# Optimization experiments

Hardware: AMD Instinct MI355X
Metric: run time of the kernel (lower is better)

## Reference

```python
import jax, jax.numpy as jnp
import numpy as np

COMMIT_WEIGHT = 0.25  # cfg.commit_weight


def setup_inputs() -> dict:
    key = jax.random.key(0)
    k1, k2 = jax.random.split(key)
    z = jax.random.normal(k1, (262144, 64), dtype=jnp.float32)
    codebook = jax.random.normal(k2, (512, 64), dtype=jnp.float32) * 0.02
    return {"z": z, "codebook": codebook}


def reference(z, codebook):
    # projector = Identity (apply_sim_vq=False)
    # squared euclidean distances [N, K]; argmin matches cdist(p=2) argmin
    d2 = (
        jnp.sum(z * z, axis=-1, keepdims=True)
        - 2.0 * (z @ codebook.T)
        + jnp.sum(codebook * codebook, axis=-1)
    )
    ids = jnp.argmin(d2, axis=-1)          # [N] int
    q = codebook[ids]                       # [N, D] gather
    loss = (
        jnp.mean((jax.lax.stop_gradient(z) - q) ** 2)
        + COMMIT_WEIGHT * jnp.mean((jax.lax.stop_gradient(q) - z) ** 2)
    )
    # straight-through estimator (training path)
    q_ste = z + jax.lax.stop_gradient(q - z)
    return q_ste, loss, ids
```

## Files before the change

kernel.cpp:

```cpp
#include <hip/hip_runtime.h>
#include <math.h>


constexpr int D     = 64;
constexpr int D4    = 16;
constexpr int K     = 512;
constexpr float STH = 2e-4f;

typedef __attribute__((ext_vector_type(8)))  short s16x8;
typedef __attribute__((ext_vector_type(16))) float f32x16;

#define FMA4(acc, zz, cc) do { \
  acc = fmaf((zz).x, (cc).x, acc); \
  acc = fmaf((zz).y, (cc).y, acc); \
  acc = fmaf((zz).z, (cc).z, acc); \
  acc = fmaf((zz).w, (cc).w, acc); } while (0)

#define MFMA_B(A, B, C) __builtin_amdgcn_mfma_f32_32x32x16_bf16(A, B, C, 0, 0, 0)

__device__ __forceinline__ unsigned short f2bf(float f) {
  unsigned u = __float_as_uint(f);
  return (unsigned short)((u + 0x7FFFu + ((u >> 16) & 1u)) >> 16);
}


#define LDS_FRAGS(CH, CL, T) do { \
  const int fb_ = (T) * 4096 + h * 512 + col * 16; \
  CH[0] = *(const s16x8*)(smem + fb_); \
  CH[1] = *(const s16x8*)(smem + fb_ + 1024); \
  CH[2] = *(const s16x8*)(smem + fb_ + 2048); \
  CH[3] = *(const s16x8*)(smem + fb_ + 3072); \
  CL[0] = *(const s16x8*)(smem + 65536 + fb_); \
  CL[1] = *(const s16x8*)(smem + 65536 + fb_ + 1024); \
  CL[2] = *(const s16x8*)(smem + 65536 + fb_ + 2048); \
  CL[3] = *(const s16x8*)(smem + 65536 + fb_ + 3072); \
} while (0)

#define LDS_GG(G, T) do { \
  const int gb_ = 131072 + (((T) * 32 + h * 16) << 2); \
  G[0] = *(const float4*)(smem + gb_); \
  G[1] = *(const float4*)(smem + gb_ + 16); \
  G[2] = *(const float4*)(smem + gb_ + 32); \
  G[3] = *(const float4*)(smem + gb_ + 48); \
} while (0)

#define TILE_BODY(T, CH, CL, G) do { \
  f32x16 acc0, acc1 = {};             \
  acc0[0]  = G[0].x; acc0[1]  = G[0].y; acc0[2]  = G[0].z; acc0[3]  = G[0].w; \
  acc0[4]  = G[1].x; acc0[5]  = G[1].y; acc0[6]  = G[1].z; acc0[7]  = G[1].w; \
  acc0[8]  = G[2].x; acc0[9]  = G[2].y; acc0[10] = G[2].z; acc0[11] = G[2].w; \
  acc0[12] = G[3].x; acc0[13] = G[3].y; acc0[14] = G[3].z; acc0[15] = G[3].w; \
  acc0 = MFMA_B(CH[0], zh[0], acc0);  acc1 = MFMA_B(CH[1], zh[1], acc1); \
  acc0 = MFMA_B(CH[2], zh[2], acc0);  acc1 = MFMA_B(CH[3], zh[3], acc1); \
  acc0 = MFMA_B(CH[0], zl[0], acc0);  acc1 = MFMA_B(CH[1], zl[1], acc1); \
  acc0 = MFMA_B(CH[2], zl[2], acc0);  acc1 = MFMA_B(CH[3], zl[3], acc1); \
  acc0 = MFMA_B(CL[0], zh[0], acc0);  acc1 = MFMA_B(CL[1], zh[1], acc1); \
  acc0 = MFMA_B(CL[2], zh[2], acc0);  acc1 = MFMA_B(CL[3], zh[3], acc1); \
   \
  float m1a = -INFINITY, m2a = -INFINITY, m1b = -INFINITY, m2b = -INFINITY; \
  int ra_ = 0, rb_ = 8; \
  _Pragma("unroll") \
  for (int r = 0; r < 8; ++r) { \
    float v = acc0[r] + acc1[r];        \
    bool gt = v > m1a;                  \
    m2a = fminf(fmaxf(v, m2a), m1a);    \
    if (gt) ra_ = r; \
    m1a = gt ? v : m1a; \
  } \
  _Pragma("unroll") \
  for (int r = 8; r < 16; ++r) { \
    float v = acc0[r] + acc1[r]; \
    bool gt = v > m1b; \
    m2b = fminf(fmaxf(v, m2b), m1b); \
    if (gt) rb_ = r; \
    m1b = gt ? v : m1b; \
  } \
   \
  float tm1 = fmaxf(m1a, m1b); \
  float tm2 = fmaxf(fminf(m1a, m1b), fmaxf(m2a, m2b)); \
  int   tr_ = (m1b > m1a) ? rb_ : ra_;    \
  bool tgt = tm1 > m1;                    \
  m2 = fmaxf(fminf(tm1, m1), fmaxf(tm2, m2)); \
  if (tgt) { rbest = tr_; tbest = (T); } \
  m1 = tgt ? tm1 : m1; \
} while (0)

__global__ __launch_bounds__(512, 2)
void vq_main(const float* __restrict__ z, const float* __restrict__ cbk,
             float* __restrict__ out, float* __restrict__ lossAcc,
             unsigned* __restrict__ done, int N)
{
  extern __shared__ char smem[];

  const int tid  = threadIdx.x;
  const int lane = tid & 63;
  const int wave = tid >> 6;
  const int col  = lane & 31;
  const int h    = lane >> 5;

  {
    const int cw = tid;
    const float4* c4 = (const float4*)(cbk + (size_t)cw * D);
    float4 f[16];
    #pragma unroll
    for (int i = 0; i < D4; ++i) f[i] = c4[i];
    float c2 = 0.f;
    #pragma unroll
    for (int i = 0; i < D4; ++i) FMA4(c2, f[i], f[i]);
    float e[64];
    #pragma unroll
    for (int i = 0; i < D4; ++i) {
      e[4*i] = f[i].x; e[4*i+1] = f[i].y; e[4*i+2] = f[i].z; e[4*i+3] = f[i].w;
    }
    const int T = cw >> 5, cc = cw & 31;
    #pragma unroll
    for (int sl = 0; sl < 4; ++sl) {
      #pragma unroll
      for (int h2 = 0; h2 < 2; ++h2) {
        const int ld0 = sl * 16 + h2 * 8;
        s16x8 vh, vl;
        #pragma unroll
        for (int j = 0; j < 8; ++j) {
          unsigned short hb = f2bf(e[ld0 + j]);
          float hf = __uint_as_float((unsigned)hb << 16);
          vh[j] = (short)hb;
          vl[j] = (short)f2bf(e[ld0 + j] - hf);
        }
        const int a = T * 4096 + sl * 1024 + h2 * 512 + cc * 16;
        *(s16x8*)(smem + a) = vh;
        *(s16x8*)(smem + 65536 + a) = vl;
      }
    }
    const int ai = (T << 5) + (((cc >> 2) & 1) << 4) + ((cc >> 3) << 2) + (cc & 3);
    *(float*)(smem + 131072 + ai * 4) = -0.5f * c2;
  }
  __syncthreads();

  float lacc = 0.f;

  #pragma unroll 1
  for (int it = 0; it < 4; ++it) {
    const long rowg = (long)blockIdx.x * 1024 + it * 256 + wave * 32 + col;

    const float4* zp4 = (const float4*)(z + (size_t)rowg * D);
    s16x8 zh[4], zl[4];
    #pragma unroll
    for (int s = 0; s < 4; ++s) {
      float4 p0 = zp4[4 * s + 2 * h];
      float4 p1 = zp4[4 * s + 2 * h + 1];
      float e[8] = {p0.x, p0.y, p0.z, p0.w, p1.x, p1.y, p1.z, p1.w};
      #pragma unroll
      for (int j = 0; j < 8; ++j) {
        unsigned short hb = f2bf(e[j]);
        float hf = __uint_as_float((unsigned)hb << 16);
        zh[s][j] = (short)hb;
        zl[s][j] = (short)f2bf(e[j] - hf);
      }
    }

    float m1 = -INFINITY, m2 = -INFINITY;
    int rbest = 0, tbest = 0;

    s16x8 chA[4], clA[4], chB[4], clB[4];
    float4 gA[4], gB[4];
    LDS_FRAGS(chA, clA, 0);  LDS_GG(gA, 0);
    LDS_FRAGS(chB, clB, 1);  LDS_GG(gB, 1);
    #pragma unroll 1
    for (int t = 0; t < 14; t += 2) {
      TILE_BODY(t, chA, clA, gA);
      LDS_FRAGS(chA, clA, t + 2);  LDS_GG(gA, t + 2);
      TILE_BODY(t + 1, chB, clB, gB);
      LDS_FRAGS(chB, clB, t + 3);  LDS_GG(gB, t + 3);
    }
    TILE_BODY(14, chA, clA, gA);
    TILE_BODY(15, chB, clB, gB);

    int idx = (tbest << 5) + (h << 2) + (rbest & 3) + ((rbest >> 2) << 3);

    float om1  = __shfl_xor(m1, 32);
    float om2  = __shfl_xor(m2, 32);
    int   oidx = __shfl_xor(idx, 32);
    float nm2 = fmaxf(fminf(m1, om1), fmaxf(m2, om2));
    bool take = (om1 > m1) || ((om1 == m1) && (oidx < idx));
    if (take) { m1 = om1; idx = oidx; }
    m2 = nm2;

    const bool certain = (m1 - m2 > STH);
    if (certain) {
      const float4* qp = (const float4*)(cbk + (size_t)idx * D) + (h << 3);
      const float4* zp = (const float4*)(z + (size_t)rowg * D) + (h << 3);
      float4*       op = (float4*)(out + (size_t)rowg * D) + (h << 3);
      #pragma unroll
      for (int i = 0; i < 8; ++i) {
        float4 q = qp[i], zz = zp[i], u, qs;
        u.x = q.x - zz.x; u.y = q.y - zz.y; u.z = q.z - zz.z; u.w = q.w - zz.w;
        qs.x = zz.x + u.x; qs.y = zz.y + u.y; qs.z = zz.z + u.z; qs.w = zz.w + u.w;
        FMA4(lacc, u, u);
        op[i] = qs;
      }
      if (h == 0) (out + (size_t)N * D + 1)[rowg] = (float)idx;
    }

    unsigned mask32 = (unsigned)__ballot((!certain) && h == 0);
    while (mask32) {
      const int c = __builtin_ctz(mask32);
      mask32 &= mask32 - 1;
      const size_t r0 = (size_t)blockIdx.x * 1024 + it * 256 + wave * 32 + c;
      const float4* zp = (const float4*)(z + r0 * D);
      float4 z0[D4];
      #pragma unroll
      for (int i = 0; i < D4; ++i) z0[i] = zp[i];
      float z2 = 0.f;
      #pragma unroll
      for (int i = 0; i < D4; ++i) FMA4(z2, z0[i], z0[i]);

      float best = INFINITY;
      int   bi = 0;
      #pragma unroll 1
      for (int j = 0; j < 8; ++j) {
        const int k = (lane << 3) + j;
        const float4* c4 = (const float4*)(cbk + (size_t)k * D);
        float4 cr[D4];
        #pragma unroll
        for (int i = 0; i < D4; ++i) cr[i] = c4[i];
        float c2 = 0.f;
        #pragma unroll
        for (int i = 0; i < D4; ++i) FMA4(c2, cr[i], cr[i]);
        float a0 = 0.f, b0 = 0.f;
        #pragma unroll
        for (int i = 0; i < 8; ++i) {
          FMA4(a0, z0[2 * i],     cr[2 * i]);
          FMA4(b0, z0[2 * i + 1], cr[2 * i + 1]);
        }
        float dot = a0 + b0;
        float d = fmaf(-2.f, dot, z2) + c2;
        if (d < best) { best = d; bi = k; }
      }

      #pragma unroll
      for (int off = 32; off > 0; off >>= 1) {
        float ob = __shfl_xor(best, off, 64);
        int  obi = __shfl_xor(bi, off, 64);
        if (ob < best || (ob == best && obi < bi)) { best = ob; bi = obi; }
      }

      if (lane == 0) {
        const float4* qp = (const float4*)(cbk + (size_t)bi * D);
        float4* o = (float4*)(out + r0 * D);
        #pragma unroll
        for (int i = 0; i < D4; ++i) {
          float4 q = qp[i], zz = z0[i], u, qs;
          u.x = q.x - zz.x; u.y = q.y - zz.y; u.z = q.z - zz.z; u.w = q.w - zz.w;
          qs.x = zz.x + u.x; qs.y = zz.y + u.y; qs.z = zz.z + u.z; qs.w = zz.w + u.w;
          FMA4(lacc, u, u);
          o[i] = qs;
        }
        (out + (size_t)N * D + 1)[r0] = (float)bi;
      }
    }
  }

  #pragma unroll
  for (int off = 32; off > 0; off >>= 1) lacc += __shfl_down(lacc, off, 64);
  if (lane == 0) atomicAdd(lossAcc, lacc);
  __syncthreads();
  if (tid == 0) {
    __threadfence();
    unsigned d = atomicAdd(done, 1u);
    if (d == gridDim.x - 1) {
      float total = atomicAdd(lossAcc, 0.0f);
      out[(size_t)N * D] = 1.25f * (total / (float)((long)N * D));
    }
  }
}

extern "C" void kernel_launch(void* const* d_in, const int* in_sizes, int n_in,
                              void* d_out, int out_size, void* d_ws, size_t ws_size,
                              hipStream_t stream)
{
  const float* z   = (const float*)d_in[0];
  const float* cbk = (const float*)d_in[1];
  float* out = (float*)d_out;
  float* ws  = (float*)d_ws;
  const int N = in_sizes[0] / D;

  float*    lossAcc = ws;
  unsigned* done    = (unsigned*)(ws + 1);

  hipMemsetAsync(ws, 0, 8, stream);
  vq_main<<<N / 1024, 512, 133120, stream>>>(z, cbk, out, lossAcc, done, N);
}
```

Baseline: 225.7 us.

## Defer uncertain rows to a separate exact-fallback kernel via global worklist

Rows whose top-two bf16 MFMA distance margin is too small are no longer re-scored inline by the wave that found them. Their indices go into a global list through an atomic counter. A second kernel then spreads exact fp32 rescoring of those rows evenly across all waves and does the final loss normalization. This is meant to remove serialized, divergent per-wave fallback loops that stall the main MFMA kernel and cause load imbalance. In exchange it adds a second launch, atomic contention on the counter, and a dependency on how many rows fall into the fallback path.

```diff
diff --git a/kernel.cpp b/kernel.cpp
--- a/kernel.cpp
+++ b/kernel.cpp
@@ -85,10 +85,10 @@
   m1 = tgt ? tm1 : m1; \
 } while (0)
 
-__global__ __launch_bounds__(512, 2)
+__global__ __launch_bounds__(512)
 void vq_main(const float* __restrict__ z, const float* __restrict__ cbk,
              float* __restrict__ out, float* __restrict__ lossAcc,
-             unsigned* __restrict__ done, int N)
+             unsigned* __restrict__ cnt, unsigned* __restrict__ list, int N)
 {
   extern __shared__ char smem[];
 
@@ -185,8 +185,7 @@
     if (take) { m1 = om1; idx = oidx; }
     m2 = nm2;
 
-    const bool certain = (m1 - m2 > STH);
-    if (certain) {
+    if (m1 - m2 > STH) {
       const float4* qp = (const float4*)(cbk + (size_t)idx * D) + (h << 3);
       const float4* zp = (const float4*)(z + (size_t)rowg * D) + (h << 3);
       float4*       op = (float4*)(out + (size_t)rowg * D) + (h << 3);
@@ -199,72 +198,95 @@
         op[i] = qs;
       }
       if (h == 0) (out + (size_t)N * D + 1)[rowg] = (float)idx;
-    }
-
-    unsigned mask32 = (unsigned)__ballot((!certain) && h == 0);
-    while (mask32) {
-      const int c = __builtin_ctz(mask32);
-      mask32 &= mask32 - 1;
-      const size_t r0 = (size_t)blockIdx.x * 1024 + it * 256 + wave * 32 + c;
-      const float4* zp = (const float4*)(z + r0 * D);
-      float4 z0[D4];
-      #pragma unroll
-      for (int i = 0; i < D4; ++i) z0[i] = zp[i];
-      float z2 = 0.f;
-      #pragma unroll
-      for (int i = 0; i < D4; ++i) FMA4(z2, z0[i], z0[i]);
-
-      float best = INFINITY;
-      int   bi = 0;
-      #pragma unroll 1
-      for (int j = 0; j < 8; ++j) {
-        const int k = (lane << 3) + j;
-        const float4* c4 = (const float4*)(cbk + (size_t)k * D);
-        float4 cr[D4];
-        #pragma unroll
-        for (int i = 0; i < D4; ++i) cr[i] = c4[i];
-        float c2 = 0.f;
-        #pragma unroll
-        for (int i = 0; i < D4; ++i) FMA4(c2, cr[i], cr[i]);
-        float a0 = 0.f, b0 = 0.f;
-        #pragma unroll
-        for (int i = 0; i < 8; ++i) {
-          FMA4(a0, z0[2 * i],     cr[2 * i]);
-          FMA4(b0, z0[2 * i + 1], cr[2 * i + 1]);
-        }
-        float dot = a0 + b0;
-        float d = fmaf(-2.f, dot, z2) + c2;
-        if (d < best) { best = d; bi = k; }
-      }
-
-      #pragma unroll
-      for (int off = 32; off > 0; off >>= 1) {
-        float ob = __shfl_xor(best, off, 64);
-        int  obi = __shfl_xor(bi, off, 64);
-        if (ob < best || (ob == best && obi < bi)) { best = ob; bi = obi; }
-      }
-
-      if (lane == 0) {
-        const float4* qp = (const float4*)(cbk + (size_t)bi * D);
-        float4* o = (float4*)(out + r0 * D);
-        #pragma unroll
-        for (int i = 0; i < D4; ++i) {
-          float4 q = qp[i], zz = z0[i], u, qs;
-          u.x = q.x - zz.x; u.y = q.y - zz.y; u.z = q.z - zz.z; u.w = q.w - zz.w;
-          qs.x = zz.x + u.x; qs.y = zz.y + u.y; qs.z = zz.z + u.z; qs.w = zz.w + u.w;
-          FMA4(lacc, u, u);
-          o[i] = qs;
-        }
-        (out + (size_t)N * D + 1)[r0] = (float)bi;
-      }
+    } else if (h == 0) {
+      unsigned p = atomicAdd(cnt, 1u);
+      list[p] = (unsigned)rowg;
     }
   }
 
   #pragma unroll
   for (int off = 32; off > 0; off >>= 1) lacc += __shfl_down(lacc, off, 64);
   if (lane == 0) atomicAdd(lossAcc, lacc);
+}
+
+__global__ __launch_bounds__(256)
+void vq_fb(const float* __restrict__ z, const float* __restrict__ cbk,
+           float* __restrict__ out, float* __restrict__ lossAcc,
+           const unsigned* __restrict__ list, const unsigned* __restrict__ cntp,
+           unsigned* __restrict__ done, int N)
+{
+  const unsigned cnt = *cntp;
+  const int tid  = threadIdx.x;
+  const int lane = tid & 63;
+  const unsigned wid = (blockIdx.x * blockDim.x + tid) >> 6;
+  const unsigned nw  = (gridDim.x * blockDim.x) >> 6;
+
+  float lacc = 0.f;
+  #pragma unroll 1
+  for (unsigned p = wid; p < cnt; p += nw) {
+    const size_t r0 = (size_t)list[p];
+
+    const float4* zp = (const float4*)(z + r0 * D);
+    float4 z0[D4];
+    #pragma unroll
+    for (int i = 0; i < D4; ++i) z0[i] = zp[i];
+    float z2 = 0.f;
+    #pragma unroll
+    for (int i = 0; i < D4; ++i) FMA4(z2, z0[i], z0[i]);
+
+    float best = INFINITY;
+    int   bi = 0;
+    #pragma unroll 1
+    for (int j = 0; j < 8; ++j) {
+      const int k = (lane << 3) + j;
+      const float4* c4 = (const float4*)(cbk + (size_t)k * D);
+      float4 cr[D4];
+      #pragma unroll
+      for (int i = 0; i < D4; ++i) cr[i] = c4[i];
+      float c2 = 0.f;
+      #pragma unroll
+      for (int i = 0; i < D4; ++i) FMA4(c2, cr[i], cr[i]);
+      float a0 = 0.f, b0 = 0.f;
+      #pragma unroll
+      for (int i = 0; i < 8; ++i) {
+        FMA4(a0, z0[2 * i],     cr[2 * i]);
+        FMA4(b0, z0[2 * i + 1], cr[2 * i + 1]);
+      }
+      float dot = a0 + b0;
+      float d = fmaf(-2.f, dot, z2) + c2;
+      if (d < best) { best = d; bi = k; }
+    }
+
+    #pragma unroll
+    for (int off = 32; off > 0; off >>= 1) {
+      float ob = __shfl_xor(best, off, 64);
+      int  obi = __shfl_xor(bi, off, 64);
+      if (ob < best || (ob == best && obi < bi)) { best = ob; bi = obi; }
+    }
+
+    if (lane == 0) {
+      const float4* qp = (const float4*)(cbk + (size_t)bi * D);
+      float4* o = (float4*)(out + r0 * D);
+      #pragma unroll
+      for (int i = 0; i < D4; ++i) {
+        float4 q = qp[i], zz = z0[i], u, qs;
+        u.x = q.x - zz.x; u.y = q.y - zz.y; u.z = q.z - zz.z; u.w = q.w - zz.w;
+        qs.x = zz.x + u.x; qs.y = zz.y + u.y; qs.z = zz.z + u.z; qs.w = zz.w + u.w;
+        FMA4(lacc, u, u);
+        o[i] = qs;
+      }
+      (out + (size_t)N * D + 1)[r0] = (float)bi;
+    }
+  }
+
+  #pragma unroll
+  for (int off = 32; off > 0; off >>= 1) lacc += __shfl_down(lacc, off, 64);
+  __shared__ float wsum[4];
+  if (lane == 0) wsum[tid >> 6] = lacc;
   __syncthreads();
   if (tid == 0) {
+    float s = wsum[0] + wsum[1] + wsum[2] + wsum[3];
+    if (s != 0.f) atomicAdd(lossAcc, s);
     __threadfence();
     unsigned d = atomicAdd(done, 1u);
     if (d == gridDim.x - 1) {
@@ -285,8 +307,11 @@
   const int N = in_sizes[0] / D;
 
   float*    lossAcc = ws;
-  unsigned* done    = (unsigned*)(ws + 1);
-
-  hipMemsetAsync(ws, 0, 8, stream);
-  vq_main<<<N / 1024, 512, 133120, stream>>>(z, cbk, out, lossAcc, done, N);
+  unsigned* cnt     = (unsigned*)(ws + 1);
+  unsigned* done    = (unsigned*)(ws + 2);
+  unsigned* list    = (unsigned*)(ws + 64);
+
+  hipMemsetAsync(ws, 0, 12, stream);
+  vq_main<<<N / 1024, 512, 133120, stream>>>(z, cbk, out, lossAcc, cnt, list, N);
+  vq_fb<<<512, 256, 0, stream>>>(z, cbk, out, lossAcc, list, cnt, done, N);
 }
```

New measurement: 218.9 us. 3.0% less time.
